# Kernel optimization log

Hardware: AMD Instinct MI355X
Metric: run time of the kernel (lower is better)

The kernel has to match this reference:

```python
import jax, jax.numpy as jnp
import numpy as np

TOP_K = 2


def setup_inputs() -> dict:
    key = jax.random.key(0)
    k0, k1, k2, k3, k4 = jax.random.split(key, 5)
    B, S, H, I, E = 4, 2048, 1024, 2816, 8
    s_h = 1.0 / np.sqrt(H)
    s_i = 1.0 / np.sqrt(I)
    return {
        "x": jax.random.normal(k0, (B, S, H), jnp.float32),
        # nn.Linear weights are stored as [out_features, in_features]
        "w_router": jax.random.normal(k1, (E, H), jnp.float32) * s_h,   # gate: H -> E
        "w_gate": jax.random.normal(k2, (E, I, H), jnp.float32) * s_h,  # per-expert gate_proj
        "w_up": jax.random.normal(k3, (E, I, H), jnp.float32) * s_h,    # per-expert up_proj
        "w_down": jax.random.normal(k4, (E, H, I), jnp.float32) * s_i,  # per-expert down_proj
    }


def reference(x, w_router, w_gate, w_up, w_down):
    B, S, H = x.shape
    E = w_router.shape[0]
    xf = x.reshape(-1, H)                      # [T, H], T = B*S

    # --- Router: softmax over experts, top-k, renormalize weights ---
    logits = jnp.einsum("th,eh->te", xf, w_router)        # [T, E]
    probs = jax.nn.softmax(logits, axis=-1)
    topw, topi = jax.lax.top_k(probs, TOP_K)              # [T, k]
    topw = topw / jnp.sum(topw, axis=-1, keepdims=True)

    # Per-token combine weight for each expert: sum_k w[t,k] * 1[idx[t,k]==e]
    onehot = (topi[..., None] == jnp.arange(E)).astype(x.dtype)  # [T, k, E]
    combine = jnp.einsum("tk,tke->te", topw, onehot)             # [T, E]

    # --- Experts: SwiGLU MLP per expert on all tokens, masked combine ---
    # (masked-dense in the original == gather-compute mathematically,
    # since silu(0)*0 = 0 and the projections have no bias)
    gate = jax.nn.silu(jnp.einsum("th,eih->eti", xf, w_gate))    # [E, T, I]
    up = jnp.einsum("th,eih->eti", xf, w_up)                     # [E, T, I]
    down = jnp.einsum("eti,ehi->eth", gate * up, w_down)         # [E, T, H]

    out = jnp.einsum("eth,te->th", down, combine)                # [T, H]
    return out.reshape(B, S, H)
```

## Files before the change

### kernel.cpp

```cpp
#include <hip/hip_runtime.h>

#define TT 8192
#define HD 1024
#define ID 2816
#define NE 8
#define NID2 (2*ID)

typedef __attribute__((ext_vector_type(8))) short short8;
typedef __attribute__((ext_vector_type(4))) float f32x4;

#define WS_TOP2I 0
#define WS_TOP2W 65536
#define WS_CNT   131072
#define WS_OFF   131136
#define WS_CUR   131200
#define WS_TMAP  131328
#define WS_SLOTW 196864
#define WS_T2S   262400
#define WS_XB    1048576ULL
#define WS_WGU   (WS_XB  + 16777216ULL)
#define WS_WDB   (WS_WGU + 92274688ULL)
#define WS_ACT   (WS_WDB + 46137344ULL)

__device__ __forceinline__ unsigned int pack_bf2(float lo, float hi) {
  unsigned int ul = __builtin_bit_cast(unsigned int, lo) + 0x8000u;
  unsigned int uh = __builtin_bit_cast(unsigned int, hi) + 0x8000u;
  return (uh & 0xffff0000u) | (ul >> 16);
}

__device__ __forceinline__ unsigned short f2bf(float f) {
  unsigned int u = __builtin_bit_cast(unsigned int, f);
  return (unsigned short)((u + 0x8000u) >> 16);
}

__device__ __forceinline__ void gload16(const void* g, void* l) {
  __builtin_amdgcn_global_load_lds(
      (const __attribute__((address_space(1))) unsigned int*)g,
      (__attribute__((address_space(3))) unsigned int*)l, 16, 0, 0);
}

__global__ __launch_bounds__(256) void router_kernel(
    const float* __restrict__ x, const float* __restrict__ wr,
    int* __restrict__ top2i, float* __restrict__ top2w,
    unsigned short* __restrict__ xb)
{
  int tid  = threadIdx.x;
  int lane = tid & 63;
  int t    = blockIdx.x * 4 + (tid >> 6);

  const float4* xp = (const float4*)(x + (size_t)t * HD + lane * 16);
  float4 xv[4];
  #pragma unroll
  for (int j = 0; j < 4; ++j) xv[j] = xp[j];

  uint4 v0, v1;
  v0.x = pack_bf2(xv[0].x, xv[0].y); v0.y = pack_bf2(xv[0].z, xv[0].w);
  v0.z = pack_bf2(xv[1].x, xv[1].y); v0.w = pack_bf2(xv[1].z, xv[1].w);
  v1.x = pack_bf2(xv[2].x, xv[2].y); v1.y = pack_bf2(xv[2].z, xv[2].w);
  v1.z = pack_bf2(xv[3].x, xv[3].y); v1.w = pack_bf2(xv[3].z, xv[3].w);
  uint4* xrow = (uint4*)(xb + (size_t)t * HD + lane * 16);
  xrow[0] = v0; xrow[1] = v1;

  float acc[NE];
  #pragma unroll
  for (int e = 0; e < NE; ++e) {
    const float4* wp = (const float4*)(wr + (size_t)e * HD + lane * 16);
    float s = 0.f;
    #pragma unroll
    for (int j = 0; j < 4; ++j) {
      float4 w = wp[j];
      s += xv[j].x * w.x + xv[j].y * w.y + xv[j].z * w.z + xv[j].w * w.w;
    }
    acc[e] = s;
  }
  #pragma unroll
  for (int d = 1; d < 64; d <<= 1) {
    #pragma unroll
    for (int e = 0; e < NE; ++e) acc[e] += __shfl_xor(acc[e], d, 64);
  }
  int   i0 = 0; float m0 = acc[0];
  #pragma unroll
  for (int e = 1; e < NE; ++e) if (acc[e] > m0) { m0 = acc[e]; i0 = e; }
  int   i1 = -1; float m1 = -3.4e38f;
  #pragma unroll
  for (int e = 0; e < NE; ++e) if (e != i0 && acc[e] > m1) { m1 = acc[e]; i1 = e; }

  float e1 = __expf(m1 - m0);
  float w0 = 1.f / (1.f + e1);
  float w1 = e1 * w0;

  if (lane == 0) {
    top2i[2 * t] = i0;  top2i[2 * t + 1] = i1;
    top2w[2 * t] = w0;  top2w[2 * t + 1] = w1;
  }
}

__global__ __launch_bounds__(256) void count_scan_kernel(
    const int* __restrict__ top2i,
    int* __restrict__ counts, int* __restrict__ offsets, int* __restrict__ cursors)
{
  __shared__ int s_cnt[NE];
  int tid = threadIdx.x;
  if (tid < NE) s_cnt[tid] = 0;
  __syncthreads();

  int c0=0,c1=0,c2=0,c3=0,c4=0,c5=0,c6=0,c7=0;
  for (int t = tid; t < TT; t += 256) {
    int e0 = top2i[2 * t], e1 = top2i[2 * t + 1];
    c0 += __popcll(__ballot(e0 == 0)) + __popcll(__ballot(e1 == 0));
    c1 += __popcll(__ballot(e0 == 1)) + __popcll(__ballot(e1 == 1));
    c2 += __popcll(__ballot(e0 == 2)) + __popcll(__ballot(e1 == 2));
    c3 += __popcll(__ballot(e0 == 3)) + __popcll(__ballot(e1 == 3));
    c4 += __popcll(__ballot(e0 == 4)) + __popcll(__ballot(e1 == 4));
    c5 += __popcll(__ballot(e0 == 5)) + __popcll(__ballot(e1 == 5));
    c6 += __popcll(__ballot(e0 == 6)) + __popcll(__ballot(e1 == 6));
    c7 += __popcll(__ballot(e0 == 7)) + __popcll(__ballot(e1 == 7));
  }
  if ((tid & 63) == 0) {
    atomicAdd(&s_cnt[0], c0); atomicAdd(&s_cnt[1], c1);
    atomicAdd(&s_cnt[2], c2); atomicAdd(&s_cnt[3], c3);
    atomicAdd(&s_cnt[4], c4); atomicAdd(&s_cnt[5], c5);
    atomicAdd(&s_cnt[6], c6); atomicAdd(&s_cnt[7], c7);
  }
  __syncthreads();
  if (tid == 0) {
    int run = 0;
    #pragma unroll
    for (int e = 0; e < NE; ++e) {
      counts[e] = s_cnt[e]; offsets[e] = run; cursors[e] = run; run += s_cnt[e];
    }
    offsets[NE] = run;
  }
}

__global__ __launch_bounds__(256) void place_kernel(
    const int* __restrict__ top2i, const float* __restrict__ top2w,
    int* __restrict__ cursors,
    int* __restrict__ token_map, float* __restrict__ slot_w, int* __restrict__ tok2slot)
{
  int tid  = threadIdx.x;
  int lane = tid & 63;
  int t    = blockIdx.x * 256 + tid;

  #pragma unroll
  for (int k = 0; k < 2; ++k) {
    int   e = top2i[2 * t + k];
    float w = top2w[2 * t + k];
    #pragma unroll
    for (int ee = 0; ee < NE; ++ee) {
      unsigned long long m = __ballot(e == ee);
      if (e == ee) {
        int leader = __ffsll((long long)m) - 1;
        int pre    = __popcll(m & ((1ull << lane) - 1ull));
        int base   = 0;
        if (lane == leader) base = atomicAdd(&cursors[ee], (int)__popcll(m));
        base = __shfl(base, leader, 64);
        token_map[base + pre] = t;
        slot_w[base + pre]    = w;
        tok2slot[2 * t + k]   = base + pre;
      }
    }
  }
}

__global__ __launch_bounds__(256) void cvt_wgu_kernel(
    const float* __restrict__ wg, const float* __restrict__ wu,
    unsigned short* __restrict__ wgu)
{
  int e   = blockIdx.y;
  int idx = blockIdx.x * 256 + threadIdx.x;
  int col8 = idx & 127;
  int rr   = idx >> 7;
  int blk  = rr >> 8;
  int win  = rr & 255;
  const float* srow = (win < 128)
      ? wg + ((size_t)e * ID + blk * 128 + win) * HD
      : wu + ((size_t)e * ID + blk * 128 + (win - 128)) * HD;
  const float4* p = (const float4*)(srow + col8 * 8);
  float4 a = p[0], b = p[1];
  uint4 v;
  v.x = pack_bf2(a.x, a.y); v.y = pack_bf2(a.z, a.w);
  v.z = pack_bf2(b.x, b.y); v.w = pack_bf2(b.z, b.w);
  *(uint4*)(wgu + ((size_t)e * NID2 + rr) * HD + col8 * 8) = v;
}

__global__ __launch_bounds__(256) void cvt_bf16_kernel(
    const float* __restrict__ in, unsigned short* __restrict__ out, int n8)
{
  int i = blockIdx.x * 256 + threadIdx.x;
  if (i >= n8) return;
  const float4* p = (const float4*)(in + (size_t)i * 8);
  float4 a = p[0], b = p[1];
  uint4 v;
  v.x = pack_bf2(a.x, a.y); v.y = pack_bf2(a.z, a.w);
  v.z = pack_bf2(b.x, b.y); v.w = pack_bf2(b.z, b.w);
  ((uint4*)out)[i] = v;
}


#define ISSUE2(t1, j0, j1, SRC, DOFF) { \
    size_t k1 = (size_t)((t1) * 64); \
    char* db = ldsc + (((t1) & 1) ? 65536u : 0u) + (unsigned)tid * 16 + (DOFF); \
    gload16(SRC[j0] + k1, db + (j0) * 8192); \
    gload16(SRC[j1] + k1, db + (j1) * 8192); }

#define ISSUE_B01(t1) ISSUE2(t1, 0, 1, bS, 32768u)
#define ISSUE_B23(t1) ISSUE2(t1, 2, 3, bS, 32768u)
#define ISSUE_A02(t1) ISSUE2(t1, 0, 2, aS, 0u)
#define ISSUE_A13(t1) ISSUE2(t1, 1, 3, aS, 0u)

#define MFMA16(MBASE) \
    __builtin_amdgcn_s_setprio(1); \
    _Pragma("unroll") for (int m = 0; m < 4; ++m) \
      _Pragma("unroll") for (int n = 0; n < 4; ++n) \
        acc[(MBASE) + m][n] = __builtin_amdgcn_mfma_f32_16x16x32_bf16(af[m], bfr[n], acc[(MBASE) + m][n], 0, 0, 0); \
    __builtin_amdgcn_s_setprio(0);

#define KTILE(t, ISSUE, N1STR) { \
    const char* sa = ldsc + (((t) & 1) ? 65536u : 0u); \
    const char* sb = sa + 32768; \
    short8 bfr[4], af[4]; \
     \
    asm volatile("s_waitcnt vmcnt(2)" ::: "memory"); \
    __builtin_amdgcn_s_barrier(); \
    if (ISSUE) ISSUE_B01((t) + 1); \
    _Pragma("unroll") for (int n = 0; n < 4; ++n) \
      bfr[n] = *(const short8*)(sb + (wc * 64 + n * 16 + arow) * 128 + (kq ^ rxor)); \
    _Pragma("unroll") for (int m = 0; m < 4; ++m) \
      af[m] = *(const short8*)(sa + (wr * 128 + m * 16 + arow) * 128 + (kq ^ rxor)); \
    MFMA16(0) \
     \
    asm volatile("s_waitcnt vmcnt(" N1STR ")" ::: "memory"); \
    __builtin_amdgcn_s_barrier(); \
    if (ISSUE) ISSUE_B23((t) + 1); \
    _Pragma("unroll") for (int m = 0; m < 4; ++m) \
      af[m] = *(const short8*)(sa + (wr * 128 + 64 + m * 16 + arow) * 128 + (kq ^ rxor)); \
    MFMA16(4) \
     \
    if (ISSUE) ISSUE_A02((t) + 1); \
    _Pragma("unroll") for (int n = 0; n < 4; ++n) \
      bfr[n] = *(const short8*)(sb + (wc * 64 + n * 16 + arow) * 128 + ((64 + kq) ^ rxor)); \
    _Pragma("unroll") for (int m = 0; m < 4; ++m) \
      af[m] = *(const short8*)(sa + (wr * 128 + m * 16 + arow) * 128 + ((64 + kq) ^ rxor)); \
    MFMA16(0) \
     \
    if (ISSUE) ISSUE_A13((t) + 1); \
    _Pragma("unroll") for (int m = 0; m < 4; ++m) \
      af[m] = *(const short8*)(sa + (wr * 128 + 64 + m * 16 + arow) * 128 + ((64 + kq) ^ rxor)); \
    MFMA16(4) }

#define XCD_DECODE(NX, NY) \
  int nwg  = (NX) * (NY) * NE; \
  int flat = blockIdx.x + (NX) * (blockIdx.y + (NY) * blockIdx.z); \
  int qq   = nwg >> 3; \
  int wg   = (flat & 7) * qq + (flat >> 3); \
  int bx   = wg % (NX); \
  int rem  = wg / (NX); \
  int y    = rem % (NY); \
  int e    = rem / (NY);

__global__ __launch_bounds__(512, 2) void gemm1_fast(
    const unsigned short* __restrict__ xb, const unsigned short* __restrict__ wgu,
    const int* __restrict__ counts, const int* __restrict__ offsets,
    const int* __restrict__ token_map, unsigned short* __restrict__ act)
{
  extern __shared__ char smem[];
  char* ldsc = smem;

  XCD_DECODE(8, 22)
  int cnt = counts[e];
  int off = offsets[e];

  int tid  = threadIdx.x;
  int lane = tid & 63;
  int w    = tid >> 6;
  int wr   = w >> 2;
  int wc   = w & 3;

  int srow0 = tid >> 3;
  int colE  = (((tid & 7) ^ ((tid >> 3) & 7)) << 3);
  int rxor  = (lane & 7) << 4;
  int arow  = lane & 15;
  int kq    = (lane >> 4) << 4;
  int prow  = (lane >> 4) << 2;

  for (int t0 = bx * 256; t0 < cnt; t0 += 2048) {
    const unsigned short* aS[4];
    const unsigned short* bS[4];
    #pragma unroll
    for (int j = 0; j < 4; ++j) {
      int row  = srow0 + 64 * j;
      int tr   = t0 + row;
      int slot = off + (tr < cnt ? tr : cnt - 1);
      aS[j] = xb  + (size_t)token_map[slot] * HD + colE;
      bS[j] = wgu + ((size_t)e * NID2 + (size_t)y * 256 + row) * HD + colE;
    }

    f32x4 zf = {0.f, 0.f, 0.f, 0.f};
    f32x4 acc[8][4];
    #pragma unroll
    for (int m = 0; m < 8; ++m)
      #pragma unroll
      for (int n = 0; n < 4; ++n) acc[m][n] = zf;

    ISSUE_B01(0); ISSUE_B23(0); ISSUE_A02(0); ISSUE_A13(0);
    for (int t = 0; t < HD / 64 - 1; ++t) KTILE(t, true, "2");
    KTILE(HD / 64 - 1, false, "0");

    __syncthreads();
    float* xch = (float*)smem;
    if (wc >= 2) {
      float* base = xch + (size_t)((wr * 2 + (wc - 2)) * 8192);
      #pragma unroll
      for (int m = 0; m < 8; ++m)
        #pragma unroll
        for (int n = 0; n < 4; ++n)
          #pragma unroll
          for (int r = 0; r < 4; ++r)
            base[(m * 16 + prow + r) * 64 + n * 16 + arow] = acc[m][n][r];
    }
    __syncthreads();
    if (wc < 2) {
      const float* base = xch + (size_t)((wr * 2 + wc) * 8192);
      int i0 = y * 128 + wc * 64;
      #pragma unroll
      for (int m = 0; m < 8; ++m) {
        #pragma unroll
        for (int r = 0; r < 4; ++r) {
          int row = wr * 128 + m * 16 + prow + r;
          int tr2 = t0 + row;
          if (tr2 >= cnt) continue;
          size_t ob = (size_t)(off + tr2) * ID + i0 + arow;
          #pragma unroll
          for (int n = 0; n < 4; ++n) {
            float g = acc[m][n][r];
            float u = base[(m * 16 + prow + r) * 64 + n * 16 + arow];
            float h = g * u / (1.f + __expf(-g));
            act[ob + n * 16] = f2bf(h);
          }
        }
      }
    }
    __syncthreads();
  }
}

__global__ __launch_bounds__(512, 2) void gemm2_fast(
    const unsigned short* __restrict__ act, const unsigned short* __restrict__ wdb,
    const int* __restrict__ counts, const int* __restrict__ offsets,
    float* __restrict__ down)
{
  extern __shared__ char smem[];
  char* ldsc = smem;

  XCD_DECODE(8, 4)
  int cnt = counts[e];
  int off = offsets[e];

  int tid  = threadIdx.x;
  int lane = tid & 63;
  int w    = tid >> 6;
  int wr   = w >> 2;
  int wc   = w & 3;

  int srow0 = tid >> 3;
  int colE  = (((tid & 7) ^ ((tid >> 3) & 7)) << 3);
  int rxor  = (lane & 7) << 4;
  int arow  = lane & 15;
  int kq    = (lane >> 4) << 4;
  int prow  = (lane >> 4) << 2;

  for (int t0 = bx * 256; t0 < cnt; t0 += 2048) {
    const unsigned short* aS[4];
    const unsigned short* bS[4];
    #pragma unroll
    for (int j = 0; j < 4; ++j) {
      int row  = srow0 + 64 * j;
      int tr   = t0 + row;
      int slot = off + (tr < cnt ? tr : cnt - 1);
      aS[j] = act + (size_t)slot * ID + colE;
      bS[j] = wdb + ((size_t)e * HD + (size_t)y * 256 + row) * ID + colE;
    }

    f32x4 zf = {0.f, 0.f, 0.f, 0.f};
    f32x4 acc[8][4];
    #pragma unroll
    for (int m = 0; m < 8; ++m)
      #pragma unroll
      for (int n = 0; n < 4; ++n) acc[m][n] = zf;

    ISSUE_B01(0); ISSUE_B23(0); ISSUE_A02(0); ISSUE_A13(0);
    for (int t = 0; t < ID / 64 - 1; ++t) KTILE(t, true, "2");
    KTILE(ID / 64 - 1, false, "0");

    #pragma unroll
    for (int m = 0; m < 8; ++m) {
      #pragma unroll
      for (int r = 0; r < 4; ++r) {
        int row = wr * 128 + m * 16 + prow + r;
        int tr2 = t0 + row;
        if (tr2 >= cnt) continue;
        float* ob = down + (size_t)(off + tr2) * HD + (size_t)y * 256 + wc * 64 + arow;
        #pragma unroll
        for (int n = 0; n < 4; ++n)
          ob[n * 16] = acc[m][n][r];
      }
    }
    __syncthreads();
  }
}

__global__ __launch_bounds__(256) void combine_kernel(
    const float* __restrict__ down, const float* __restrict__ slot_w,
    const int* __restrict__ tok2slot, float* __restrict__ out)
{
  int t   = blockIdx.x;
  int tid = threadIdx.x;
  int s0  = tok2slot[2 * t], s1 = tok2slot[2 * t + 1];
  float w0 = slot_w[s0], w1 = slot_w[s1];
  const float4* d0 = (const float4*)(down + (size_t)s0 * HD) + tid;
  const float4* d1 = (const float4*)(down + (size_t)s1 * HD) + tid;
  float4 a = *d0, b = *d1;
  float4 o;
  o.x = w0 * a.x + w1 * b.x;  o.y = w0 * a.y + w1 * b.y;
  o.z = w0 * a.z + w1 * b.z;  o.w = w0 * a.w + w1 * b.w;
  ((float4*)(out + (size_t)t * HD))[tid] = o;
}

extern "C" void kernel_launch(void* const* d_in, const int* in_sizes, int n_in,
                              void* d_out, int out_size, void* d_ws, size_t ws_size,
                              hipStream_t stream) {
  const float* x        = (const float*)d_in[0];
  const float* w_router = (const float*)d_in[1];
  const float* w_gate   = (const float*)d_in[2];
  const float* w_up     = (const float*)d_in[3];
  const float* w_down   = (const float*)d_in[4];

  char* ws = (char*)d_ws;
  int*   top2i    = (int*)(ws + WS_TOP2I);
  float* top2w    = (float*)(ws + WS_TOP2W);
  int*   counts   = (int*)(ws + WS_CNT);
  int*   offsets  = (int*)(ws + WS_OFF);
  int*   cursors  = (int*)(ws + WS_CUR);
  int*   tmap     = (int*)(ws + WS_TMAP);
  float* slotw    = (float*)(ws + WS_SLOTW);
  int*   tok2slot = (int*)(ws + WS_T2S);
  unsigned short* xb  = (unsigned short*)(ws + WS_XB);
  unsigned short* wgu = (unsigned short*)(ws + WS_WGU);
  unsigned short* wdb = (unsigned short*)(ws + WS_WDB);
  unsigned short* act = (unsigned short*)(ws + WS_ACT);
  float*          down = (float*)(ws + WS_WGU);

  hipFuncSetAttribute((const void*)gemm1_fast,
                      hipFuncAttributeMaxDynamicSharedMemorySize, 131072);
  hipFuncSetAttribute((const void*)gemm2_fast,
                      hipFuncAttributeMaxDynamicSharedMemorySize, 131072);

  router_kernel<<<TT / 4, 256, 0, stream>>>(x, w_router, top2i, top2w, xb);
  count_scan_kernel<<<1, 256, 0, stream>>>(top2i, counts, offsets, cursors);
  place_kernel<<<TT / 256, 256, 0, stream>>>(top2i, top2w, cursors, tmap, slotw, tok2slot);
  cvt_wgu_kernel<<<dim3(2816, NE), 256, 0, stream>>>(w_gate, w_up, wgu);
  cvt_bf16_kernel<<<11264, 256, 0, stream>>>(w_down, wdb, NE * HD * ID / 8);

  gemm1_fast<<<dim3(8, 22, NE), 512, 131072, stream>>>(xb, wgu, counts, offsets, tmap, act);
  gemm2_fast<<<dim3(8, 4, NE), 512, 131072, stream>>>(act, wdb, counts, offsets, down);
  combine_kernel<<<TT, 256, 0, stream>>>(down, slotw, tok2slot, (float*)d_out);
}
```

Measured before the change: 564.8 us.

## Restructure GEMM k-loop into ping-pong barrier schedule with deeper prefetch

Rewrites the k-tile macro so each quarter-tile issues its LDS reads, then a global prefetch, then barrier-bracketed MFMA bursts, in a ping-pong style where waves alternate between memory and compute phases. The B01 half of the tile two steps ahead is now prefetched early, so global loads run further ahead of use. It also drops the min-2-blocks occupancy hint from the launch bounds, allowing more registers per thread. The cost is more barriers per tile and possibly lower occupancy.

```diff
diff --git a/kernel.cpp b/kernel.cpp
--- a/kernel.cpp
+++ b/kernel.cpp
@@ -198,56 +198,58 @@
 }
 
 
-#define ISSUE2(t1, j0, j1, SRC, DOFF) { \
-    size_t k1 = (size_t)((t1) * 64); \
-    char* db = ldsc + (((t1) & 1) ? 65536u : 0u) + (unsigned)tid * 16 + (DOFF); \
-    gload16(SRC[j0] + k1, db + (j0) * 8192); \
-    gload16(SRC[j1] + k1, db + (j1) * 8192); }
-
-#define ISSUE_B01(t1) ISSUE2(t1, 0, 1, bS, 32768u)
-#define ISSUE_B23(t1) ISSUE2(t1, 2, 3, bS, 32768u)
-#define ISSUE_A02(t1) ISSUE2(t1, 0, 2, aS, 0u)
-#define ISSUE_A13(t1) ISSUE2(t1, 1, 3, aS, 0u)
-
-#define MFMA16(MBASE) \
+#define VW2() asm volatile("s_waitcnt vmcnt(2)" ::: "memory")
+#define VW0() asm volatile("s_waitcnt vmcnt(0)" ::: "memory")
+#define LG0() asm volatile("s_waitcnt lgkmcnt(0)" ::: "memory")
+#define BAR() __builtin_amdgcn_s_barrier()
+
+#define DBUF(u) (ldsc + (((u) & 1) ? 65536u : 0u) + (unsigned)tid * 16)
+#define ISS_B01(u) { size_t k1 = (size_t)((u) * 64); char* db = DBUF(u); \
+    gload16(bS[0] + k1, db + 32768); gload16(bS[1] + k1, db + 40960); }
+#define ISS_B23(u) { size_t k1 = (size_t)((u) * 64); char* db = DBUF(u); \
+    gload16(bS[2] + k1, db + 49152); gload16(bS[3] + k1, db + 57344); }
+#define ISS_A02(u) { size_t k1 = (size_t)((u) * 64); char* db = DBUF(u); \
+    gload16(aS[0] + k1, db);         gload16(aS[2] + k1, db + 16384); }
+#define ISS_A13(u) { size_t k1 = (size_t)((u) * 64); char* db = DBUF(u); \
+    gload16(aS[1] + k1, db + 8192);  gload16(aS[3] + k1, db + 24576); }
+
+#define RD_B(KB) \
+    _Pragma("unroll") for (int n = 0; n < 4; ++n) \
+      bfr[n] = *(const short8*)(sB + (wc * 64 + n * 16 + arow) * 128 + ((KB) ^ rxor));
+#define RD_A(MH, KB) \
+    _Pragma("unroll") for (int m = 0; m < 4; ++m) \
+      af[m] = *(const short8*)(sa + (wr * 128 + (MH) * 64 + m * 16 + arow) * 128 + ((KB) ^ rxor));
+#define MF(MB) \
     __builtin_amdgcn_s_setprio(1); \
     _Pragma("unroll") for (int m = 0; m < 4; ++m) \
       _Pragma("unroll") for (int n = 0; n < 4; ++n) \
-        acc[(MBASE) + m][n] = __builtin_amdgcn_mfma_f32_16x16x32_bf16(af[m], bfr[n], acc[(MBASE) + m][n], 0, 0, 0); \
+        acc[(MB) + m][n] = __builtin_amdgcn_mfma_f32_16x16x32_bf16(af[m], bfr[n], acc[(MB) + m][n], 0, 0, 0); \
     __builtin_amdgcn_s_setprio(0);
 
-#define KTILE(t, ISSUE, N1STR) { \
+#define KTILE(t, NT) { \
     const char* sa = ldsc + (((t) & 1) ? 65536u : 0u); \
-    const char* sb = sa + 32768; \
+    const char* sB = sa + 32768; \
     short8 bfr[4], af[4]; \
-     \
-    asm volatile("s_waitcnt vmcnt(2)" ::: "memory"); \
-    __builtin_amdgcn_s_barrier(); \
-    if (ISSUE) ISSUE_B01((t) + 1); \
-    _Pragma("unroll") for (int n = 0; n < 4; ++n) \
-      bfr[n] = *(const short8*)(sb + (wc * 64 + n * 16 + arow) * 128 + (kq ^ rxor)); \
-    _Pragma("unroll") for (int m = 0; m < 4; ++m) \
-      af[m] = *(const short8*)(sa + (wr * 128 + m * 16 + arow) * 128 + (kq ^ rxor)); \
-    MFMA16(0) \
-     \
-    asm volatile("s_waitcnt vmcnt(" N1STR ")" ::: "memory"); \
-    __builtin_amdgcn_s_barrier(); \
-    if (ISSUE) ISSUE_B23((t) + 1); \
-    _Pragma("unroll") for (int m = 0; m < 4; ++m) \
-      af[m] = *(const short8*)(sa + (wr * 128 + 64 + m * 16 + arow) * 128 + (kq ^ rxor)); \
-    MFMA16(4) \
-     \
-    if (ISSUE) ISSUE_A02((t) + 1); \
-    _Pragma("unroll") for (int n = 0; n < 4; ++n) \
-      bfr[n] = *(const short8*)(sb + (wc * 64 + n * 16 + arow) * 128 + ((64 + kq) ^ rxor)); \
-    _Pragma("unroll") for (int m = 0; m < 4; ++m) \
-      af[m] = *(const short8*)(sa + (wr * 128 + m * 16 + arow) * 128 + ((64 + kq) ^ rxor)); \
-    MFMA16(0) \
-     \
-    if (ISSUE) ISSUE_A13((t) + 1); \
-    _Pragma("unroll") for (int m = 0; m < 4; ++m) \
-      af[m] = *(const short8*)(sa + (wr * 128 + 64 + m * 16 + arow) * 128 + ((64 + kq) ^ rxor)); \
-    MFMA16(4) }
+    int u1 = (t) + 1, u2 = (t) + 2; \
+     RD_B(kq) RD_A(0, kq) \
+    if (u1 < (NT)) ISS_B23(u1); \
+    BAR(); LG0(); MF(0) BAR(); \
+     RD_A(1, kq) \
+    if (u1 < (NT)) ISS_A02(u1); \
+    BAR(); LG0(); MF(4) BAR(); \
+     RD_B(64 + kq) RD_A(0, 64 + kq) \
+    if (u1 < (NT)) ISS_A13(u1); \
+    BAR(); LG0(); MF(0) BAR(); \
+     RD_A(1, 64 + kq) \
+    if (u2 < (NT)) { ISS_B01(u2); VW2(); } \
+    else if (u1 < (NT)) { VW0(); } \
+    BAR(); LG0(); MF(4) BAR(); }
+
+#define KLOOP(NT) { \
+    ISS_B01(0); ISS_B23(0); ISS_A02(0); ISS_A13(0); \
+    ISS_B01(1); \
+    VW2(); BAR(); \
+    for (int t = 0; t < (NT); ++t) KTILE(t, (NT)); }
 
 #define XCD_DECODE(NX, NY) \
   int nwg  = (NX) * (NY) * NE; \
@@ -259,7 +261,7 @@
   int y    = rem % (NY); \
   int e    = rem / (NY);
 
-__global__ __launch_bounds__(512, 2) void gemm1_fast(
+__global__ __launch_bounds__(512) void gemm1_fast(
     const unsigned short* __restrict__ xb, const unsigned short* __restrict__ wgu,
     const int* __restrict__ counts, const int* __restrict__ offsets,
     const int* __restrict__ token_map, unsigned short* __restrict__ act)
@@ -303,9 +305,7 @@
       #pragma unroll
       for (int n = 0; n < 4; ++n) acc[m][n] = zf;
 
-    ISSUE_B01(0); ISSUE_B23(0); ISSUE_A02(0); ISSUE_A13(0);
-    for (int t = 0; t < HD / 64 - 1; ++t) KTILE(t, true, "2");
-    KTILE(HD / 64 - 1, false, "0");
+    KLOOP(HD / 64);
 
     __syncthreads();
     float* xch = (float*)smem;
@@ -345,7 +345,7 @@
   }
 }
 
-__global__ __launch_bounds__(512, 2) void gemm2_fast(
+__global__ __launch_bounds__(512) void gemm2_fast(
     const unsigned short* __restrict__ act, const unsigned short* __restrict__ wdb,
     const int* __restrict__ counts, const int* __restrict__ offsets,
     float* __restrict__ down)
@@ -389,9 +389,7 @@
       #pragma unroll
       for (int n = 0; n < 4; ++n) acc[m][n] = zf;
 
-    ISSUE_B01(0); ISSUE_B23(0); ISSUE_A02(0); ISSUE_A13(0);
-    for (int t = 0; t < ID / 64 - 1; ++t) KTILE(t, true, "2");
-    KTILE(ID / 64 - 1, false, "0");
+    KLOOP(ID / 64);
 
     #pragma unroll
     for (int m = 0; m < 8; ++m) {
```

New measurement: 594.1 us. 5.2% more time.
